# Optimization experiments

Hardware: AMD Instinct MI355X
Metric: run time of the kernel (lower is better)

Reference implementation:

```python
import jax, jax.numpy as jnp
import numpy as np

B, T_NEW, CACHED_MAX = 8, 128, 2048
D_MODEL, N_HEADS = 1024, 16
D_HEAD = D_MODEL // N_HEADS
MAX_TOTAL = CACHED_MAX + T_NEW


def rotate_half(x):
    x1, x2 = x[..., : x.shape[-1] // 2], x[..., x.shape[-1] // 2 :]
    return jnp.concatenate([-x2, x1], axis=-1)


def setup_inputs() -> dict:
    key = jax.random.key(0)
    ks = jax.random.split(key, 16)
    w_scale = D_MODEL ** -0.5  # xavier-ish
    inp = {
        "x_new": jax.random.normal(ks[0], (B, T_NEW, D_MODEL), jnp.float32),
        "past_k": jax.random.normal(ks[1], (B, N_HEADS, CACHED_MAX, D_HEAD), jnp.float32),
        "past_v": jax.random.normal(ks[2], (B, N_HEADS, CACHED_MAX, D_HEAD), jnp.float32),
        "Wq": jax.random.normal(ks[3], (D_MODEL, D_MODEL), jnp.float32) * w_scale,
        "bq": jnp.zeros((D_MODEL,), jnp.float32),
        "Wk": jax.random.normal(ks[4], (D_MODEL, D_MODEL), jnp.float32) * w_scale,
        "bk": jnp.zeros((D_MODEL,), jnp.float32),
        "Wv": jax.random.normal(ks[5], (D_MODEL, D_MODEL), jnp.float32) * w_scale,
        "bv": jnp.zeros((D_MODEL,), jnp.float32),
        "Wo": jax.random.normal(ks[6], (D_MODEL, D_MODEL), jnp.float32) * w_scale,
        "bo": jnp.zeros((D_MODEL,), jnp.float32),
        "inv_freq": 1.0 / (10000.0 ** (jnp.arange(0, D_HEAD, 2, dtype=jnp.float32) / D_HEAD)),
        # ragged lengths; >=1 so every row attends to something
        "past_lengths": jax.random.randint(ks[7], (B,), 1, CACHED_MAX + 1),
        "new_lengths": jax.random.randint(ks[8], (B,), 1, T_NEW + 1),
    }
    return inp


def _attention_fwd(x_new, past_k, past_v, Wq, bq, Wk, bk, Wv, bv, Wo, bo, inv_freq,
                   past_lengths, new_lengths):
    steps = jnp.arange(T_NEW)
    valid_new = steps[None, :] < new_lengths[:, None]            # [B, T_new]

    def proj(W, b):  # torch Linear: x @ W.T + b -> [B, H, T_new, D_head]
        y = jnp.einsum("btm,nm->btn", x_new, W) + b
        return y.reshape(B, T_NEW, N_HEADS, D_HEAD).transpose(0, 2, 1, 3)

    q, k_new, v_new = proj(Wq, bq), proj(Wk, bk), proj(Wv, bv)

    # RoPE at absolute positions past_len + step (0 where invalid)
    positions = jnp.where(valid_new, past_lengths[:, None] + steps[None, :], 0)
    freqs = positions[..., None].astype(jnp.float32) * inv_freq  # [B, T_new, D_head/2]
    emb = jnp.concatenate([freqs, freqs], axis=-1)               # [B, T_new, D_head]
    cos = jnp.cos(emb)[:, None]                                  # [B, 1, T_new, D_head]
    sin = jnp.sin(emb)[:, None]
    q = q * cos + rotate_half(q) * sin
    k_new = k_new * cos + rotate_half(k_new) * sin

    vm = valid_new[:, None, :, None].astype(q.dtype)
    q, k_new, v_new = q * vm, k_new * vm, v_new * vm

    total_lengths = past_lengths + new_lengths
    j = jnp.arange(MAX_TOTAL)
    in_past = (j[None, :] < past_lengths[:, None])[:, None, :, None]       # [B,1,MT,1]
    in_new = ((j[None, :] >= past_lengths[:, None]) &
              (j[None, :] < total_lengths[:, None]))[:, None, :, None]
    idx_new = jnp.clip(j[None, :] - past_lengths[:, None], 0, T_NEW - 1)   # [B, MT]

    past_k_pad = jnp.pad(past_k, ((0, 0), (0, 0), (0, T_NEW), (0, 0)))
    past_v_pad = jnp.pad(past_v, ((0, 0), (0, 0), (0, T_NEW), (0, 0)))
    gather = jax.vmap(lambda xb, ib: xb[:, ib])  # [H,T_new,D], [MT] -> [H,MT,D]
    k_total = jnp.where(in_past, past_k_pad, jnp.where(in_new, gather(k_new, idx_new), 0.0))
    v_total = jnp.where(in_past, past_v_pad, jnp.where(in_new, gather(v_new, idx_new), 0.0))

    attend = j[None, :] < total_lengths[:, None]                  # [B, MT]
    scores = jnp.einsum("bhqd,bhkd->bhqk", q, k_total) * (D_HEAD ** -0.5)
    neg = jnp.asarray(jnp.finfo(scores.dtype).min, scores.dtype)
    scores = jnp.where(attend[:, None, None, :], scores, neg)
    attn = jax.nn.softmax(scores, axis=-1)
    ctx = jnp.einsum("bhqk,bhkd->bhqd", attn, v_total)            # [B,H,T_new,D]

    out = ctx.transpose(0, 2, 1, 3).reshape(B, T_NEW, D_MODEL)
    out = jnp.einsum("btm,nm->btn", out, Wo) + bo
    return out * valid_new[..., None].astype(out.dtype)


def reference(x_new, past_k, past_v, Wq, bq, Wk, bk, Wv, bv, Wo, bo, inv_freq,
              past_lengths, new_lengths):
    return _attention_fwd(x_new, past_k, past_v, Wq, bq, Wk, bk, Wv, bv, Wo, bo,
                          inv_freq, past_lengths, new_lengths)
```

## Files before the change

### kernel.cpp

```cpp
#include <hip/hip_runtime.h>

#define NB 8
#define TNEW 128
#define CMAX 2048
#define DMODEL 1024
#define NH 16
#define DH 64

typedef float f32x4 __attribute__((ext_vector_type(4)));
typedef short short8 __attribute__((ext_vector_type(8)));
typedef short short4v __attribute__((ext_vector_type(4)));
typedef unsigned uint4v __attribute__((ext_vector_type(4)));

__device__ __forceinline__ short f2bf(float x) {
  unsigned u = __float_as_uint(x);
  u += 0x7FFFu + ((u >> 16) & 1u);
  return (short)(u >> 16);
}
__device__ __forceinline__ float bf2f(short s) {
  return __uint_as_float(((unsigned)(unsigned short)s) << 16);
}
__device__ __forceinline__ short8 cvt8(f32x4 a, f32x4 b) {
  uint4v t;
  asm("v_cvt_pk_bf16_f32 %0, %1, %2" : "=v"(t.x) : "v"(a.x), "v"(a.y));
  asm("v_cvt_pk_bf16_f32 %0, %1, %2" : "=v"(t.y) : "v"(a.z), "v"(a.w));
  asm("v_cvt_pk_bf16_f32 %0, %1, %2" : "=v"(t.z) : "v"(b.x), "v"(b.y));
  asm("v_cvt_pk_bf16_f32 %0, %1, %2" : "=v"(t.w) : "v"(b.z), "v"(b.w));
  return __builtin_bit_cast(short8, t);
}

#define LGKM0_BAR()                                            \
  __builtin_amdgcn_sched_barrier(0);                           \
  asm volatile("s_waitcnt lgkmcnt(0)" ::: "memory");           \
  __builtin_amdgcn_sched_barrier(0);                           \
  __builtin_amdgcn_s_barrier()
#define TAIL_BAR()                                             \
  __builtin_amdgcn_sched_barrier(0);                           \
  __builtin_amdgcn_s_barrier()

__global__ __launch_bounds__(256) void cvt5_bf16(
    const float* __restrict__ s0, const float* __restrict__ s1,
    const float* __restrict__ s2, const float* __restrict__ s3,
    const float* __restrict__ s4, short* __restrict__ dst) {
  const int seg = blockIdx.x >> 10;
  const int i = (blockIdx.x & 1023) * 256 + threadIdx.x;
  const float* src = seg == 0 ? s0 : seg == 1 ? s1 : seg == 2 ? s2 : seg == 3 ? s3 : s4;
  f32x4 v = *(const f32x4*)(src + (size_t)i * 4);
  short4v o;
  o.x = f2bf(v.x); o.y = f2bf(v.y); o.z = f2bf(v.z); o.w = f2bf(v.w);
  *(short4v*)(dst + (size_t)seg * (1u << 20) + (size_t)i * 4) = o;
}

template<int MODE>
__global__ __launch_bounds__(256) void gemm64(
    const short* __restrict__ A, const short* __restrict__ Wbase,
    void* __restrict__ Out, const float* __restrict__ bias0,
    const float* __restrict__ bias1, const float* __restrict__ bias2,
    const int* __restrict__ new_len, const float* __restrict__ inv_freq,
    const int* __restrict__ past_len)
{
  constexpr int LDT = 40;
  __shared__ short As[64 * LDT];
  __shared__ short Bs[64 * LDT];
  const int n0 = blockIdx.x * 64, m0 = blockIdx.y * 64, z = blockIdx.z;
  if (MODE == 0 && (m0 & 64) && new_len[m0 >> 7] <= 64) return;
  const short* Wp = Wbase + (size_t)z * (DMODEL * DMODEL);
  const float* bias = (MODE == 0) ? (z == 0 ? bias0 : (z == 1 ? bias1 : bias2)) : bias0;
  const int tid = threadIdx.x, lane = tid & 63, w = tid >> 6;
  const int wm = (w >> 1) * 32, wn2 = (w & 1) * 16;
  const int lr = lane & 15, lk = lane >> 4;

  const int srow = tid >> 2, soff = (tid & 3) * 8;
  const short* Ag = A  + (size_t)(m0 + srow) * DMODEL + soff;
  const short* Bg = Wp + (size_t)(n0 + srow) * DMODEL + soff;
  short* Al = As + srow * LDT + soff;
  short* Bl = Bs + srow * LDT + soff;

  short8 va0 = *(const short8*)(Ag);
  short8 vb0 = *(const short8*)(Bg);
  short8 va1, vb1;
  f32x4 acc[2][2] = {};

#define GEMM_PHASE(CURA, CURB, NXTA, NXTB, KNEXT)                          \
  {                                                                        \
    *(short8*)Al = CURA;                                                   \
    *(short8*)Bl = CURB;                                                   \
    NXTA = *(const short8*)(Ag + (KNEXT) * 32);                            \
    NXTB = *(const short8*)(Bg + (KNEXT) * 32);                            \
    LGKM0_BAR();                                                           \
    short8 af0 = *(const short8*)(As + (wm + lr) * LDT + lk * 8);          \
    short8 af1 = *(const short8*)(As + (wm + 16 + lr) * LDT + lk * 8);     \
    short8 bg0 = *(const short8*)(Bs + (wn2 + lr) * LDT + lk * 8);         \
    short8 bg1 = *(const short8*)(Bs + (wn2 + 32 + lr) * LDT + lk * 8);    \
    acc[0][0] = __builtin_amdgcn_mfma_f32_16x16x32_bf16(af0, bg0, acc[0][0], 0, 0, 0); \
    acc[0][1] = __builtin_amdgcn_mfma_f32_16x16x32_bf16(af0, bg1, acc[0][1], 0, 0, 0); \
    acc[1][0] = __builtin_amdgcn_mfma_f32_16x16x32_bf16(af1, bg0, acc[1][0], 0, 0, 0); \
    acc[1][1] = __builtin_amdgcn_mfma_f32_16x16x32_bf16(af1, bg1, acc[1][1], 0, 0, 0); \
    TAIL_BAR();                                                            \
  }

  for (int kt = 0; kt < DMODEL / 32; kt += 2) {
    const int k1 = kt + 1;
    const int k2 = (kt + 2 < DMODEL / 32) ? kt + 2 : DMODEL / 32 - 1;
    GEMM_PHASE(va0, vb0, va1, vb1, k1);
    GEMM_PHASE(va1, vb1, va0, vb0, k2);
  }
#undef GEMM_PHASE

  const int colb = n0 + wn2 + lr;
  const float b0 = bias[colb], b1 = bias[colb + 32];

  if (MODE == 0 && z <= 1) {
    const int bb = m0 >> 7;
    const int pbase = past_len[bb];
    const float fr = inv_freq[(wn2 + lr) & 31];
    short* outp = (short*)Out + (size_t)z * (NB * TNEW * DMODEL);
#pragma unroll
    for (int i = 0; i < 2; ++i) {
#pragma unroll
      for (int r = 0; r < 4; ++r) {
        const int row = m0 + wm + i * 16 + lk * 4 + r;
        const float pos = (float)(pbase + (row & 127));
        float sn, cs;
        sincosf(pos * fr, &sn, &cs);
        const float a0 = acc[i][0][r] + b0;
        const float a1 = acc[i][1][r] + b1;
        outp[(size_t)row * DMODEL + colb]      = f2bf(a0 * cs - a1 * sn);
        outp[(size_t)row * DMODEL + colb + 32] = f2bf(a1 * cs + a0 * sn);
      }
    }
  } else {
#pragma unroll
    for (int i = 0; i < 2; ++i) {
#pragma unroll
      for (int r = 0; r < 4; ++r) {
        const int row = m0 + wm + i * 16 + lk * 4 + r;
        const float a0 = acc[i][0][r] + b0;
        const float a1 = acc[i][1][r] + b1;
        if (MODE == 0) {
          short* outp = (short*)Out + (size_t)z * (NB * TNEW * DMODEL);
          outp[(size_t)row * DMODEL + colb]      = f2bf(a0);
          outp[(size_t)row * DMODEL + colb + 32] = f2bf(a1);
        } else {
          const int bb = row >> 7, t = row & 127;
          const bool ok = t < new_len[bb];
          ((float*)Out)[(size_t)row * DMODEL + colb]      = ok ? a0 : 0.0f;
          ((float*)Out)[(size_t)row * DMODEL + colb + 32] = ok ? a1 : 0.0f;
        }
      }
    }
  }
}

__global__ __launch_bounds__(512, 4) void attn_split(
    const float* __restrict__ pk, const float* __restrict__ pv,
    const short* __restrict__ qb, const short* __restrict__ kb,
    const short* __restrict__ vb, float* __restrict__ Opart,
    float* __restrict__ Ml, const int* __restrict__ past_len,
    const int* __restrict__ new_len, int splits)
{
  constexpr int LDT = 72;
  __shared__ short Kl[64 * LDT];
  __shared__ short Vt[64 * LDT];
  __shared__ short Pl[128 * LDT];
  const int id = blockIdx.x;
  const int bh = id / splits, s = id - bh * splits;
  const int b = bh >> 4, h = bh & 15;
  const int past = past_len[b];
  const int nlen = new_len[b];
  const int total = past + nlen;
  const int tid = threadIdx.x, lane = tid & 63, w = tid >> 6;
  const int lr = lane & 15, lk = lane >> 4;

  const int nt = (total + 63) >> 6;

  float* mlp = Ml + (size_t)(bh * splits + s) * 256;
  float* op  = Opart + (size_t)(bh * splits + s) * (128 * 64);

  if (s >= nt) {
#pragma unroll
    for (int r = 0; r < 4; ++r) {
      const int q = w * 16 + lk * 4 + r;
      if (lr == 0) { mlp[q] = -3.0e38f; mlp[128 + q] = 0.f; }
    }
    return;
  }

  const bool wvalid = (w * 16) < nlen;
  short8 qf0 = {}, qf1 = {};
  if (wvalid) {
    const short* qrow = qb + (size_t)(b * 128 + w * 16 + lr) * DMODEL + h * 64;
    qf0 = *(const short8*)(qrow + lk * 8);
    qf1 = *(const short8*)(qrow + 32 + lk * 8);
  }
  float m_run[4], l_run[4];
  f32x4 acc[4] = {};
#pragma unroll
  for (int r = 0; r < 4; ++r) { m_run[r] = -3.0e38f; l_run[r] = 0.f; }

  const int jr = tid >> 3, seg = tid & 7;
  const float* pkb = pk + ((size_t)(b * 16 + h) * CMAX) * 64 + seg * 8;
  const float* pvb = pv + ((size_t)(b * 16 + h) * CMAX) * 64 + seg * 8;
  const short* kbb = kb + (size_t)(b * 128) * DMODEL + h * 64 + seg * 8;
  const short* vbb = vb + (size_t)(b * 128) * DMODEL + h * 64 + seg * 8;

  f32x4 kF0, kF1, vF0, vF1;
  short8 kN, vN;
  bool pr0, pr1;

#define STAGE_ISSUE(T)                                                        \
  {                                                                           \
    const int j_ = (T) * 64 + jr;                                             \
    const int jp = min(j_, past - 1);                   \
    const int jn = min(max(j_ - past, 0), TNEW - 1);                          \
    pr0 = j_ < past;                                                          \
    pr1 = j_ < total;                                                         \
    kF0 = *(const f32x4*)(pkb + (size_t)jp * 64);                             \
    kF1 = *(const f32x4*)(pkb + (size_t)jp * 64 + 4);                         \
    vF0 = *(const f32x4*)(pvb + (size_t)jp * 64);                             \
    vF1 = *(const f32x4*)(pvb + (size_t)jp * 64 + 4);                         \
    kN  = *(const short8*)(kbb + (size_t)jn * DMODEL);                        \
    vN  = *(const short8*)(vbb + (size_t)jn * DMODEL);                        \
  }

  STAGE_ISSUE(s);
  for (int kt = s; kt < nt; kt += splits) {
    {
      const short8 z8 = {};
      short8 kc = cvt8(kF0, kF1);
      short8 vc = cvt8(vF0, vF1);
      short8 kr = pr0 ? kc : (pr1 ? kN : z8);
      short8 vr = pr0 ? vc : (pr1 ? vN : z8);
      *(short8*)(Kl + jr * LDT + seg * 8) = kr;
#pragma unroll
      for (int i = 0; i < 8; ++i) Vt[(seg * 8 + i) * LDT + (jr ^ (seg * 8))] = vr[i];
    }
    STAGE_ISSUE(kt + splits);
    LGKM0_BAR();

    if (wvalid) {
      f32x4 sc[4];
      __builtin_amdgcn_s_setprio(1);
#pragma unroll
      for (int nf = 0; nf < 4; ++nf) {
        short8 k0 = *(const short8*)(Kl + (nf * 16 + lr) * LDT + lk * 8);
        short8 k1 = *(const short8*)(Kl + (nf * 16 + lr) * LDT + 32 + lk * 8);
        f32x4 zv = {};
        zv = __builtin_amdgcn_mfma_f32_16x16x32_bf16(qf0, k0, zv, 0, 0, 0);
        sc[nf] = __builtin_amdgcn_mfma_f32_16x16x32_bf16(qf1, k1, zv, 0, 0, 0);
      }
      __builtin_amdgcn_s_setprio(0);
      const int kg0 = kt * 64;
      float pmax[4] = {-3.0e38f, -3.0e38f, -3.0e38f, -3.0e38f};
#pragma unroll
      for (int nf = 0; nf < 4; ++nf) {
        const bool ok = (kg0 + nf * 16 + lr) < total;
#pragma unroll
        for (int r = 0; r < 4; ++r) {
          const float sv = ok ? sc[nf][r] * 0.125f : -3.0e38f;
          sc[nf][r] = sv;
          pmax[r] = fmaxf(pmax[r], sv);
        }
      }
#pragma unroll
      for (int r = 0; r < 4; ++r) {
#pragma unroll
        for (int off = 1; off < 16; off <<= 1)
          pmax[r] = fmaxf(pmax[r], __shfl_xor(pmax[r], off));
      }
      float alpha[4], rsum[4];
#pragma unroll
      for (int r = 0; r < 4; ++r) {
        const float mn = fmaxf(m_run[r], pmax[r]);
        alpha[r] = __expf(m_run[r] - mn);
        m_run[r] = mn;
        rsum[r] = 0.f;
      }
#pragma unroll
      for (int nf = 0; nf < 4; ++nf)
#pragma unroll
        for (int r = 0; r < 4; ++r) {
          const float p = __expf(sc[nf][r] - m_run[r]);
          sc[nf][r] = p;
          rsum[r] += p;
        }
#pragma unroll
      for (int r = 0; r < 4; ++r) {
#pragma unroll
        for (int off = 1; off < 16; off <<= 1)
          rsum[r] += __shfl_xor(rsum[r], off);
        l_run[r] = l_run[r] * alpha[r] + rsum[r];
      }
#pragma unroll
      for (int nf = 0; nf < 4; ++nf)
#pragma unroll
        for (int r = 0; r < 4; ++r) acc[nf][r] *= alpha[r];

#pragma unroll
      for (int nf = 0; nf < 4; ++nf)
#pragma unroll
        for (int r = 0; r < 4; ++r)
          Pl[(w * 16 + lk * 4 + r) * LDT + nf * 16 + lr] = f2bf(sc[nf][r]);
      __builtin_amdgcn_s_setprio(1);
#pragma unroll
      for (int kf = 0; kf < 2; ++kf) {
        short8 pf = *(const short8*)(Pl + (w * 16 + lr) * LDT + kf * 32 + lk * 8);
#pragma unroll
        for (int nf = 0; nf < 4; ++nf) {
          const int dd = nf * 16 + lr;
          short8 vf = *(const short8*)(Vt + dd * LDT + ((kf * 32 + lk * 8) ^ (dd & 56)));
          acc[nf] = __builtin_amdgcn_mfma_f32_16x16x32_bf16(pf, vf, acc[nf], 0, 0, 0);
        }
      }
      __builtin_amdgcn_s_setprio(0);
    }
    TAIL_BAR();
  }
#undef STAGE_ISSUE

  if (wvalid) {
#pragma unroll
    for (int nf = 0; nf < 4; ++nf)
#pragma unroll
      for (int r = 0; r < 4; ++r) {
        const int q = w * 16 + lk * 4 + r, d = nf * 16 + lr;
        op[(size_t)q * 64 + d] = acc[nf][r];
      }
#pragma unroll
    for (int r = 0; r < 4; ++r) {
      const int q = w * 16 + lk * 4 + r;
      if (lr == 0) { mlp[q] = m_run[r]; mlp[128 + q] = l_run[r]; }
    }
  } else {
#pragma unroll
    for (int r = 0; r < 4; ++r) {
      const int q = w * 16 + lk * 4 + r;
      if (lr == 0) { mlp[q] = -3.0e38f; mlp[128 + q] = 0.f; }
    }
  }
}

__global__ __launch_bounds__(256) void attn_combine(
    const float* __restrict__ Opart, const float* __restrict__ Ml,
    short* __restrict__ ctxb, const int* __restrict__ new_len, int splits)
{
  const int bh = blockIdx.x, b = bh >> 4, h = bh & 15;
  const int q = blockIdx.y * 16 + (threadIdx.x >> 4);
  if (q >= new_len[b]) return;
  const int dv = (threadIdx.x & 15) * 4;
  const float* mlb = Ml + (size_t)bh * splits * 256;
  float mstar = -3.0e38f;
  for (int s = 0; s < splits; ++s)
    mstar = fmaxf(mstar, mlb[s * 256 + q]);
  float lsum = 0.f;
  f32x4 o = {};
  for (int s = 0; s < splits; ++s) {
    const float ws = __expf(mlb[s * 256 + q] - mstar);
    lsum += ws * mlb[s * 256 + 128 + q];
    if (ws > 0.f) {
      f32x4 ov = *(const f32x4*)(Opart + ((size_t)(bh * splits + s) * 128 + q) * 64 + dv);
      o.x += ws * ov.x; o.y += ws * ov.y; o.z += ws * ov.z; o.w += ws * ov.w;
    }
  }
  const float inv = 1.0f / lsum;
  short4v r;
  r.x = f2bf(o.x * inv); r.y = f2bf(o.y * inv); r.z = f2bf(o.z * inv); r.w = f2bf(o.w * inv);
  *(short4v*)(ctxb + (size_t)(b * 128 + q) * DMODEL + h * 64 + dv) = r;
}

extern "C" void kernel_launch(void* const* d_in, const int* in_sizes, int n_in,
                              void* d_out, int out_size, void* d_ws, size_t ws_size,
                              hipStream_t stream) {
  const float* x      = (const float*)d_in[0];
  const float* past_k = (const float*)d_in[1];
  const float* past_v = (const float*)d_in[2];
  const float* Wq = (const float*)d_in[3];
  const float* bq = (const float*)d_in[4];
  const float* Wk = (const float*)d_in[5];
  const float* bk = (const float*)d_in[6];
  const float* Wv = (const float*)d_in[7];
  const float* bv = (const float*)d_in[8];
  const float* Wo = (const float*)d_in[9];
  const float* bo = (const float*)d_in[10];
  const float* inv_freq = (const float*)d_in[11];
  const int* past_len = (const int*)d_in[12];
  const int* new_len  = (const int*)d_in[13];

  short* wsb = (short*)d_ws;
  const size_t M1 = 1u << 20;
  short* Xb  = wsb;
  short* Wqb = wsb + 1 * M1;
  short* Wob = wsb + 4 * M1;
  short* qb  = wsb + 5 * M1;
  short* kb  = wsb + 6 * M1;
  short* vb  = wsb + 7 * M1;
  short* ctx = wsb + 8 * M1;
  float* Opart = (float*)(wsb + 9 * M1);

  int splits = 1;
  for (int s = 8; s >= 1; s >>= 1) {
    size_t need = 9 * M1 * sizeof(short) +
                  (size_t)s * 128 * (128 * 64 + 256) * sizeof(float);
    if (need <= ws_size) { splits = s; break; }
  }
  float* Ml = Opart + (size_t)128 * splits * (128 * 64);

  cvt5_bf16<<<5120, 256, 0, stream>>>(x, Wq, Wk, Wv, Wo, wsb);

  gemm64<0><<<dim3(16, 16, 3), 256, 0, stream>>>(Xb, Wqb, (void*)qb, bq, bk, bv,
                                                 new_len, inv_freq, past_len);
  attn_split<<<128 * splits, 512, 0, stream>>>(past_k, past_v, qb, kb, vb,
                                               Opart, Ml, past_len, new_len, splits);
  attn_combine<<<dim3(128, 8), 256, 0, stream>>>(Opart, Ml, ctx, new_len, splits);
  gemm64<1><<<dim3(16, 16, 1), 256, 0, stream>>>(ctx, Wob, d_out, bo, nullptr, nullptr,
                                                 new_len, nullptr, nullptr);
}
```

Measured before the change: 67.65 us.

## Rewrite QKV GEMM with 64x128 tiles, direct global-to-LDS loads and swizzle

Replaces the templated 64x64 GEMM for the QKV projection with a dedicated kernel. It uses 64x128 tiles, a K-step of 64, double-buffered LDS filled via global_load_lds with an XOR swizzle, setprio around the MFMAs, and fast __sincosf for RoPE. The output projection gets its own kernel that zero-fills padded row blocks and skips their GEMM work. The attention split count may now go up to 16 when the workspace allows. The aim is to reduce the number of LDS staging passes and barriers and to raise MFMA density, at the cost of more LDS per block and possible occupancy and workspace pressure.

```diff
diff --git a/kernel.cpp b/kernel.cpp
--- a/kernel.cpp
+++ b/kernel.cpp
@@ -28,6 +28,11 @@
   asm("v_cvt_pk_bf16_f32 %0, %1, %2" : "=v"(t.w) : "v"(b.z), "v"(b.w));
   return __builtin_bit_cast(short8, t);
 }
+__device__ __forceinline__ void gload16(const void* g, void* l) {
+  __builtin_amdgcn_global_load_lds(
+      (const __attribute__((address_space(1))) void*)g,
+      (__attribute__((address_space(3))) void*)l, 16, 0, 0);
+}
 
 #define LGKM0_BAR()                                            \
   __builtin_amdgcn_sched_barrier(0);                           \
@@ -35,6 +40,11 @@
   __builtin_amdgcn_sched_barrier(0);                           \
   __builtin_amdgcn_s_barrier()
 #define TAIL_BAR()                                             \
+  __builtin_amdgcn_sched_barrier(0);                           \
+  __builtin_amdgcn_s_barrier()
+#define VM0_BAR()                                              \
+  __builtin_amdgcn_sched_barrier(0);                           \
+  asm volatile("s_waitcnt vmcnt(0)" ::: "memory");             \
   __builtin_amdgcn_sched_barrier(0);                           \
   __builtin_amdgcn_s_barrier()
 
@@ -51,28 +61,136 @@
   *(short4v*)(dst + (size_t)seg * (1u << 20) + (size_t)i * 4) = o;
 }
 
-template<int MODE>
-__global__ __launch_bounds__(256) void gemm64(
-    const short* __restrict__ A, const short* __restrict__ Wbase,
-    void* __restrict__ Out, const float* __restrict__ bias0,
-    const float* __restrict__ bias1, const float* __restrict__ bias2,
-    const int* __restrict__ new_len, const float* __restrict__ inv_freq,
-    const int* __restrict__ past_len)
+__global__ __launch_bounds__(256) void qkv_gemm(
+    const short* __restrict__ A,
+    const short* __restrict__ W,
+    short* __restrict__ Out,
+    const float* __restrict__ bq, const float* __restrict__ bk,
+    const float* __restrict__ bv, const float* __restrict__ inv_freq,
+    const int* __restrict__ past_len, const int* __restrict__ new_len)
+{
+  __shared__ short As[2][64 * 64];
+  __shared__ short Bs[2][128 * 64];
+  const int n0 = blockIdx.x * 128;
+  const int m0 = blockIdx.y * 64;
+  const int b  = m0 >> 7;
+  if ((m0 & 64) && new_len[b] <= 64) return;
+  const int z = n0 >> 10;
+  const float* bias = z == 0 ? bq : (z == 1 ? bk : bv);
+  const int tid = threadIdx.x, lane = tid & 63, w = tid >> 6;
+  const int lr = lane & 15, lk = lane >> 4;
+  const int wm = (w >> 1) * 32, wn = (w & 1) * 64;
+
+  const int g8 = lane >> 3;
+  const int sc = ((lane & 7) ^ g8) * 8;
+
+  f32x4 acc[2][4] = {};
+
+#define QKV_STAGE(KT, BUF)                                                    \
+  {                                                                           \
+    _Pragma("unroll")                                                         \
+    for (int i = 0; i < 2; ++i) {                                             \
+      const int row = (w * 2 + i) * 8 + g8;                                   \
+      gload16(A + (size_t)(m0 + row) * DMODEL + (KT) * 64 + sc,               \
+              &As[BUF][(w * 2 + i) * 512]);                                   \
+    }                                                                         \
+    _Pragma("unroll")                                                         \
+    for (int i = 0; i < 4; ++i) {                                             \
+      const int row = (w * 4 + i) * 8 + g8;                                   \
+      gload16(W + (size_t)(n0 + row) * DMODEL + (KT) * 64 + sc,               \
+              &Bs[BUF][(w * 4 + i) * 512]);                                   \
+    }                                                                         \
+  }
+
+  QKV_STAGE(0, 0);
+  VM0_BAR();
+  for (int kt = 0; kt < 16; ++kt) {
+    const int buf = kt & 1;
+    if (kt < 15) QKV_STAGE(kt + 1, buf ^ 1);
+#pragma unroll
+    for (int ks = 0; ks < 2; ++ks) {
+      short8 af[2], bfv[4];
+#pragma unroll
+      for (int i = 0; i < 2; ++i) {
+        const int ra = wm + i * 16 + lr;
+        af[i] = *(const short8*)(&As[buf][ra * 64 + (((ks << 2) + lk) ^ (lr & 7)) * 8]);
+      }
+#pragma unroll
+      for (int j = 0; j < 4; ++j) {
+        const int rb = wn + j * 16 + lr;
+        bfv[j] = *(const short8*)(&Bs[buf][rb * 64 + (((ks << 2) + lk) ^ (lr & 7)) * 8]);
+      }
+      __builtin_amdgcn_s_setprio(1);
+#pragma unroll
+      for (int i = 0; i < 2; ++i)
+#pragma unroll
+        for (int j = 0; j < 4; ++j)
+          acc[i][j] = __builtin_amdgcn_mfma_f32_16x16x32_bf16(af[i], bfv[j], acc[i][j], 0, 0, 0);
+      __builtin_amdgcn_s_setprio(0);
+    }
+    VM0_BAR();
+  }
+#undef QKV_STAGE
+
+  const int cz = (n0 & 1023) + wn + lr;
+  const int pbase = past_len[b];
+  short* outp = Out + ((size_t)z << 20);
+  if (z <= 1) {
+#pragma unroll
+    for (int i = 0; i < 2; ++i)
+#pragma unroll
+      for (int rr = 0; rr < 4; ++rr) {
+        const int row = m0 + wm + i * 16 + lk * 4 + rr;
+        const float pos = (float)(pbase + (row & 127));
+#pragma unroll
+        for (int j = 0; j < 2; ++j) {
+          const float fr = inv_freq[j * 16 + lr];
+          float sn, cs;
+          __sincosf(pos * fr, &sn, &cs);
+          const float a0 = acc[i][j][rr]     + bias[cz + j * 16];
+          const float a1 = acc[i][j + 2][rr] + bias[cz + j * 16 + 32];
+          outp[(size_t)row * DMODEL + cz + j * 16]      = f2bf(a0 * cs - a1 * sn);
+          outp[(size_t)row * DMODEL + cz + j * 16 + 32] = f2bf(a1 * cs + a0 * sn);
+        }
+      }
+  } else {
+#pragma unroll
+    for (int i = 0; i < 2; ++i)
+#pragma unroll
+      for (int rr = 0; rr < 4; ++rr) {
+        const int row = m0 + wm + i * 16 + lk * 4 + rr;
+#pragma unroll
+        for (int j = 0; j < 4; ++j)
+          outp[(size_t)row * DMODEL + cz + j * 16] = f2bf(acc[i][j][rr] + bias[cz + j * 16]);
+      }
+  }
+}
+
+__global__ __launch_bounds__(256) void outproj64(
+    const short* __restrict__ A, const short* __restrict__ W,
+    float* __restrict__ Out, const float* __restrict__ bias,
+    const int* __restrict__ new_len)
 {
   constexpr int LDT = 40;
   __shared__ short As[64 * LDT];
   __shared__ short Bs[64 * LDT];
-  const int n0 = blockIdx.x * 64, m0 = blockIdx.y * 64, z = blockIdx.z;
-  if (MODE == 0 && (m0 & 64) && new_len[m0 >> 7] <= 64) return;
-  const short* Wp = Wbase + (size_t)z * (DMODEL * DMODEL);
-  const float* bias = (MODE == 0) ? (z == 0 ? bias0 : (z == 1 ? bias1 : bias2)) : bias0;
+  const int n0 = blockIdx.x * 64, m0 = blockIdx.y * 64;
+  const int nlen = new_len[m0 >> 7];
+  if ((m0 & 64) && nlen <= 64) {
+    const int rr = threadIdx.x >> 2, cc = (threadIdx.x & 3) * 16;
+    const f32x4 z4 = {};
+#pragma unroll
+    for (int u = 0; u < 4; ++u)
+      *(f32x4*)(&Out[(size_t)(m0 + rr) * DMODEL + n0 + cc + u * 4]) = z4;
+    return;
+  }
   const int tid = threadIdx.x, lane = tid & 63, w = tid >> 6;
   const int wm = (w >> 1) * 32, wn2 = (w & 1) * 16;
   const int lr = lane & 15, lk = lane >> 4;
 
   const int srow = tid >> 2, soff = (tid & 3) * 8;
-  const short* Ag = A  + (size_t)(m0 + srow) * DMODEL + soff;
-  const short* Bg = Wp + (size_t)(n0 + srow) * DMODEL + soff;
+  const short* Ag = A + (size_t)(m0 + srow) * DMODEL + soff;
+  const short* Bg = W + (size_t)(n0 + srow) * DMODEL + soff;
   short* Al = As + srow * LDT + soff;
   short* Bl = Bs + srow * LDT + soff;
 
@@ -109,47 +227,15 @@
 
   const int colb = n0 + wn2 + lr;
   const float b0 = bias[colb], b1 = bias[colb + 32];
-
-  if (MODE == 0 && z <= 1) {
-    const int bb = m0 >> 7;
-    const int pbase = past_len[bb];
-    const float fr = inv_freq[(wn2 + lr) & 31];
-    short* outp = (short*)Out + (size_t)z * (NB * TNEW * DMODEL);
-#pragma unroll
-    for (int i = 0; i < 2; ++i) {
-#pragma unroll
-      for (int r = 0; r < 4; ++r) {
-        const int row = m0 + wm + i * 16 + lk * 4 + r;
-        const float pos = (float)(pbase + (row & 127));
-        float sn, cs;
-        sincosf(pos * fr, &sn, &cs);
-        const float a0 = acc[i][0][r] + b0;
-        const float a1 = acc[i][1][r] + b1;
-        outp[(size_t)row * DMODEL + colb]      = f2bf(a0 * cs - a1 * sn);
-        outp[(size_t)row * DMODEL + colb + 32] = f2bf(a1 * cs + a0 * sn);
-      }
-    }
-  } else {
-#pragma unroll
-    for (int i = 0; i < 2; ++i) {
-#pragma unroll
-      for (int r = 0; r < 4; ++r) {
-        const int row = m0 + wm + i * 16 + lk * 4 + r;
-        const float a0 = acc[i][0][r] + b0;
-        const float a1 = acc[i][1][r] + b1;
-        if (MODE == 0) {
-          short* outp = (short*)Out + (size_t)z * (NB * TNEW * DMODEL);
-          outp[(size_t)row * DMODEL + colb]      = f2bf(a0);
-          outp[(size_t)row * DMODEL + colb + 32] = f2bf(a1);
-        } else {
-          const int bb = row >> 7, t = row & 127;
-          const bool ok = t < new_len[bb];
-          ((float*)Out)[(size_t)row * DMODEL + colb]      = ok ? a0 : 0.0f;
-          ((float*)Out)[(size_t)row * DMODEL + colb + 32] = ok ? a1 : 0.0f;
-        }
-      }
-    }
-  }
+#pragma unroll
+  for (int i = 0; i < 2; ++i)
+#pragma unroll
+    for (int r = 0; r < 4; ++r) {
+      const int row = m0 + wm + i * 16 + lk * 4 + r;
+      const bool ok = (row & 127) < nlen;
+      Out[(size_t)row * DMODEL + colb]      = ok ? acc[i][0][r] + b0 : 0.0f;
+      Out[(size_t)row * DMODEL + colb + 32] = ok ? acc[i][1][r] + b1 : 0.0f;
+    }
 }
 
 __global__ __launch_bounds__(512, 4) void attn_split(
@@ -398,7 +484,7 @@
   float* Opart = (float*)(wsb + 9 * M1);
 
   int splits = 1;
-  for (int s = 8; s >= 1; s >>= 1) {
+  for (int s = 16; s >= 1; s >>= 1) {
     size_t need = 9 * M1 * sizeof(short) +
                   (size_t)s * 128 * (128 * 64 + 256) * sizeof(float);
     if (need <= ws_size) { splits = s; break; }
@@ -407,11 +493,10 @@
 
   cvt5_bf16<<<5120, 256, 0, stream>>>(x, Wq, Wk, Wv, Wo, wsb);
 
-  gemm64<0><<<dim3(16, 16, 3), 256, 0, stream>>>(Xb, Wqb, (void*)qb, bq, bk, bv,
-                                                 new_len, inv_freq, past_len);
+  qkv_gemm<<<dim3(24, 16), 256, 0, stream>>>(Xb, Wqb, qb, bq, bk, bv,
+                                             inv_freq, past_len, new_len);
   attn_split<<<128 * splits, 512, 0, stream>>>(past_k, past_v, qb, kb, vb,
                                                Opart, Ml, past_len, new_len, splits);
   attn_combine<<<dim3(128, 8), 256, 0, stream>>>(Opart, Ml, ctx, new_len, splits);
-  gemm64<1><<<dim3(16, 16, 1), 256, 0, stream>>>(ctx, Wob, d_out, bo, nullptr, nullptr,
-                                                 new_len, nullptr, nullptr);
-}
+  outproj64<<<dim3(16, 16), 256, 0, stream>>>(ctx, Wob, (float*)d_out, bo, new_len);
+}
```

Result: slower. 74.07 us (+9.5%).
